# Kernel optimization log

Measured on AMD Instinct MI355X. Metric: run time of the kernel, lower is better.

## Reference

```python
import jax, jax.numpy as jnp
import numpy as np

B, H, C, N, K_TERMS = 256, 512, 64, 100, 8


def eval_cubic_spline(coeffs, tobs, t):
    # coeffs: [B, N-1, 4, C]; tobs: [N] sorted knots; t: scalar
    idx = jnp.clip(jnp.searchsorted(tobs, t, side='right') - 1, 0, tobs.shape[0] - 2)
    dt = t - tobs[idx]
    c = coeffs[:, idx]  # [B, 4, C]
    # Horner evaluation: c0 + c1*dt + c2*dt^2 + c3*dt^3
    return c[:, 0] + dt * (c[:, 1] + dt * (c[:, 2] + dt * c[:, 3]))


def setup_inputs() -> dict:
    key = jax.random.key(0)
    k_h, k_c, k_dc, k_wx, k_wh, k_wo = jax.random.split(key, 6)
    xav = lambda k, shape: jax.random.uniform(
        k, shape, minval=-1.0, maxval=1.0, dtype=jnp.float32
    ) * np.float32(np.sqrt(6.0 / (shape[0] + shape[1])))
    return {
        't': jnp.float32(0.5),
        'h': jax.random.normal(k_h, (B, H), dtype=jnp.float32),
        'coeffs': jax.random.normal(k_c, (B, N - 1, 4, C), dtype=jnp.float32),
        'dcoeffs': jax.random.normal(k_dc, (B, N - 1, 4, C), dtype=jnp.float32),
        'tobs': jnp.linspace(0.0, 1.0, N, dtype=jnp.float32),
        'wx': xav(k_wx, (H, C)),
        'wh': xav(k_wh, (H, H)),
        'wout': xav(k_wo, (H, H)),
        'b0': jnp.zeros((H,), dtype=jnp.float32),
        'b1': jnp.zeros((H,), dtype=jnp.float32),
    }


def reference(t, h, coeffs, dcoeffs, tobs, wx, wh, wout, b0, b1):
    x = eval_cubic_spline(coeffs, tobs, t)      # [B, C]
    xdot = eval_cubic_spline(dcoeffs, tobs, t)  # [B, C]
    l1 = x @ wx.T + h @ wh.T + b0               # [B, H]
    relu = jnp.maximum(l1, 0.0)
    th = jnp.tanh(relu @ wout.T + b1)           # [B, H]
    dtanh = 1.0 - th * th
    drelu = jax.nn.sigmoid(l1)                  # surrogate_relu branch
    # Jacobian assembly via broadcasted outer product: [B, H, H]
    d_outer = dtanh[:, :, None] * wout[None, :, :] * drelu[:, None, :]
    Jx = d_outer @ wx                           # [B, H, C]
    Jh = d_outer @ wh                           # [B, H, H]
    curr = jnp.einsum('bhc,bc->bh', Jx, xdot)   # jx matvec, [B, H]
    h_dot = curr
    for _ in range(K_TERMS):                    # Neumann-series recurrence
        curr = jnp.einsum('bij,bj->bi', Jh, curr)
        h_dot = h_dot + curr
    return h_dot
```

## Files before the change

### kernel.cpp

```cpp
#include <hip/hip_runtime.h>

#define BB 256
#define HH 512
#define CC 64
#define NN 100
#define KT 8

typedef short s16x8 __attribute__((ext_vector_type(8)));
typedef float f32x4 __attribute__((ext_vector_type(4)));

#define MFMA16(a, b, c) __builtin_amdgcn_mfma_f32_16x16x32_bf16((a), (b), (c), 0, 0, 0)

static __device__ __forceinline__ unsigned short f2bf(float f) {
    union { float f; unsigned int u; } v; v.f = f;
    unsigned int r = v.u + 0x7FFFu + ((v.u >> 16) & 1u);
    return (unsigned short)(r >> 16);
}


__global__ void k_pack(const float* __restrict__ wh, const float* __restrict__ wout,
                       const float* __restrict__ wx, const float* __restrict__ h,
                       const float* __restrict__ coeffs, const float* __restrict__ dcoeffs,
                       const float* __restrict__ tobs, const float* __restrict__ tg,
                       unsigned short* __restrict__ whp, unsigned short* __restrict__ wop,
                       unsigned short* __restrict__ wxp, unsigned short* __restrict__ hf,
                       unsigned short* __restrict__ xf, unsigned short* __restrict__ xdf) {
    int gid = blockIdx.x * 256 + threadIdx.x;
    if (gid < 524288) {
        const float* src = (gid < 262144) ? wh : wout;
        unsigned short* dst = (gid < 262144) ? whp : wop;
        int p = gid & 262143;
        int e = p & 7, lane = (p >> 3) & 63, g = (p >> 9) & 15, cg = (p >> 13) & 1, w = p >> 14;
        int row = w * 32 + cg * 16 + (lane & 15);
        int k = g * 32 + (lane >> 4) * 8 + e;
        dst[p] = f2bf(src[row * HH + k]);
    } else if (gid < 557056) {
        int p = gid - 524288;
        int e = p & 7, lane = (p >> 3) & 63, g = (p >> 9) & 1, cg = (p >> 10) & 1, w = p >> 11;
        int row = w * 32 + cg * 16 + (lane & 15);
        int k = g * 32 + (lane >> 4) * 8 + e;
        wxp[p] = f2bf(wx[row * CC + k]);
    } else if (gid < 688128) {
        int p = gid - 557056;
        int e = p & 7, lane = (p >> 3) & 63, g = (p >> 9) & 15, btp = p >> 13;
        int row = btp * 16 + (lane & 15);
        int k = g * 32 + (lane >> 4) * 8 + e;
        hf[p] = f2bf(h[row * HH + k]);
    } else if (gid < 704512) {
        int p = gid - 688128;
        int b = p >> 6, c = p & 63;
        float t = tg[0];
        int cntv = 0;
        for (int n = 0; n < NN; n++) cntv += (tobs[n] <= t) ? 1 : 0;
        int idx = cntv - 1;
        idx = idx < 0 ? 0 : (idx > NN - 2 ? NN - 2 : idx);
        float dt = t - tobs[idx];
        const float* cb = coeffs + ((size_t)(b * (NN - 1) + idx) * 4) * CC + c;
        float xv = cb[0] + dt * (cb[CC] + dt * (cb[2 * CC] + dt * cb[3 * CC]));
        const float* db = dcoeffs + ((size_t)(b * (NN - 1) + idx) * 4) * CC + c;
        float xd = db[0] + dt * (db[CC] + dt * (db[2 * CC] + dt * db[3 * CC]));
        int fi = (b >> 4) * 1024 + (c >> 5) * 512 + ((b & 15) + ((c >> 3) & 3) * 16) * 8 + (c & 7);
        xf[fi] = f2bf(xv);
        xdf[fi] = f2bf(xd);
    }
}

__global__ __launch_bounds__(512) void k_fused(
    const unsigned short* __restrict__ whp, const unsigned short* __restrict__ wop,
    const unsigned short* __restrict__ wxp, const unsigned short* __restrict__ hf,
    const unsigned short* __restrict__ xf, const unsigned short* __restrict__ xdf,
    const float* __restrict__ b0g, const float* __restrict__ b1g,
    float* __restrict__ outp) {
    __shared__ __align__(16) unsigned short sa[2][8192];
    const int tid = threadIdx.x;
    const int w = tid >> 6, lane = tid & 63;
    const int col2 = lane & 15, kq = lane >> 4;
    const int bt = blockIdx.x;

    float b0v[4], b1v[4];
    int fb[4];
#pragma unroll
    for (int t = 0; t < 4; t++) {
        const int c = (w * 4 + t) * 16 + col2;
        b0v[t] = b0g[c];
        b1v[t] = b1g[c];
        fb[t] = ((w * 4 + t) >> 1) * 512 + (col2 & 7) + (((t * 2 + (col2 >> 3)) & 3) << 7) + kq * 32;
    }

    const s16x8* wlh = (const s16x8*)whp + (size_t)w * 4096 + lane;
    const s16x8* wlo = (const s16x8*)wop + (size_t)w * 4096 + lane;

    float dr[4][4], dt[4][4], hd[4][4];

    {
        const s16x8* ha = (const s16x8*)(hf + (size_t)bt * 8192) + lane;
        f32x4 acc[4] = {{0.f, 0.f, 0.f, 0.f}, {0.f, 0.f, 0.f, 0.f},
                        {0.f, 0.f, 0.f, 0.f}, {0.f, 0.f, 0.f, 0.f}};
        f32x4 vac[4] = {{0.f, 0.f, 0.f, 0.f}, {0.f, 0.f, 0.f, 0.f},
                        {0.f, 0.f, 0.f, 0.f}, {0.f, 0.f, 0.f, 0.f}};
        s16x8 bfr[2][4], af[2];
        af[0] = ha[0];
#pragma unroll
        for (int t = 0; t < 4; t++) bfr[0][t] = wlh[t * 1024];
#pragma unroll
        for (int g = 0; g < 16; g++) {
            if (g < 15) {
                af[(g + 1) & 1] = ha[(g + 1) * 64];
#pragma unroll
                for (int t = 0; t < 4; t++) bfr[(g + 1) & 1][t] = wlh[t * 1024 + (g + 1) * 64];
            }
#pragma unroll
            for (int t = 0; t < 4; t++) acc[t] = MFMA16(af[g & 1], bfr[g & 1][t], acc[t]);
        }
#pragma unroll
        for (int g = 0; g < 2; g++) {
            const s16x8 xa = *((const s16x8*)(xf + (size_t)bt * 1024 + g * 512) + lane);
            const s16x8 xda = *((const s16x8*)(xdf + (size_t)bt * 1024 + g * 512) + lane);
#pragma unroll
            for (int t = 0; t < 4; t++) {
                const s16x8 bf = ((const s16x8*)wxp)[(size_t)((w * 4 + t) * 2 + g) * 64 + lane];
                acc[t] = MFMA16(xa, bf, acc[t]);
                vac[t] = MFMA16(xda, bf, vac[t]);
            }
        }
#pragma unroll
        for (int t = 0; t < 4; t++)
#pragma unroll
            for (int r = 0; r < 4; r++) {
                const float l1 = acc[t][r] + b0v[t];
                const float dra = 1.f / (1.f + expf(-l1));
                dr[t][r] = dra;
                sa[0][fb[t] + r * 8] = f2bf(fmaxf(l1, 0.f));
                sa[1][fb[t] + r * 8] = f2bf(dra * vac[t][r]);
            }
    }
    __syncthreads();

    {
        const unsigned short* A0 = &sa[0][lane * 8];
        const unsigned short* A1 = &sa[1][lane * 8];
        f32x4 acc[4] = {{0.f, 0.f, 0.f, 0.f}, {0.f, 0.f, 0.f, 0.f},
                        {0.f, 0.f, 0.f, 0.f}, {0.f, 0.f, 0.f, 0.f}};
        f32x4 cac[4] = {{0.f, 0.f, 0.f, 0.f}, {0.f, 0.f, 0.f, 0.f},
                        {0.f, 0.f, 0.f, 0.f}, {0.f, 0.f, 0.f, 0.f}};
        s16x8 bfr[2][4];
#pragma unroll
        for (int t = 0; t < 4; t++) bfr[0][t] = wlo[t * 1024];
#pragma unroll
        for (int g = 0; g < 16; g++) {
            if (g < 15) {
#pragma unroll
                for (int t = 0; t < 4; t++) bfr[(g + 1) & 1][t] = wlo[t * 1024 + (g + 1) * 64];
            }
            const s16x8 ar = *(const s16x8*)(A0 + (size_t)g * 512);
            const s16x8 as = *(const s16x8*)(A1 + (size_t)g * 512);
#pragma unroll
            for (int t = 0; t < 4; t++) {
                acc[t] = MFMA16(ar, bfr[g & 1][t], acc[t]);
                cac[t] = MFMA16(as, bfr[g & 1][t], cac[t]);
            }
        }
        __syncthreads();
#pragma unroll
        for (int t = 0; t < 4; t++)
#pragma unroll
            for (int r = 0; r < 4; r++) {
                const float th = tanhf(acc[t][r] + b1v[t]);
                const float dtv = 1.f - th * th;
                dt[t][r] = dtv;
                const float c0 = dtv * cac[t][r];
                hd[t][r] = c0;
                sa[0][fb[t] + r * 8] = f2bf(c0);
            }
    }
    __syncthreads();

    const unsigned short* A0 = &sa[0][lane * 8];
    const unsigned short* A1 = &sa[1][lane * 8];
    for (int p = 0; p < 16; p++) {
        const s16x8* wl = (p & 1) ? wlo : wlh;
        const unsigned short* Ar = (p & 1) ? A1 : A0;
        f32x4 acc[4] = {{0.f, 0.f, 0.f, 0.f}, {0.f, 0.f, 0.f, 0.f},
                        {0.f, 0.f, 0.f, 0.f}, {0.f, 0.f, 0.f, 0.f}};
        s16x8 bfr[2][4];
#pragma unroll
        for (int t = 0; t < 4; t++) bfr[0][t] = wl[t * 1024];
#pragma unroll
        for (int g = 0; g < 16; g++) {
            if (g < 15) {
#pragma unroll
                for (int t = 0; t < 4; t++) bfr[(g + 1) & 1][t] = wl[t * 1024 + (g + 1) * 64];
            }
            const s16x8 a = *(const s16x8*)(Ar + (size_t)g * 512);
#pragma unroll
            for (int t = 0; t < 4; t++) acc[t] = MFMA16(a, bfr[g & 1][t], acc[t]);
        }
        unsigned short* Aw = &sa[(p + 1) & 1][0];
        if (p & 1) {
            if (p < 15) {
#pragma unroll
                for (int t = 0; t < 4; t++)
#pragma unroll
                    for (int r = 0; r < 4; r++) {
                        float v = dt[t][r] * acc[t][r];
                        hd[t][r] += v;
                        Aw[fb[t] + r * 8] = f2bf(v);
                    }
            } else {
#pragma unroll
                for (int t = 0; t < 4; t++)
#pragma unroll
                    for (int r = 0; r < 4; r++) hd[t][r] += dt[t][r] * acc[t][r];
            }
        } else {
#pragma unroll
            for (int t = 0; t < 4; t++)
#pragma unroll
                for (int r = 0; r < 4; r++)
                    Aw[fb[t] + r * 8] = f2bf(dr[t][r] * acc[t][r]);
        }
        if (p < 15) __syncthreads();
    }

#pragma unroll
    for (int t = 0; t < 4; t++) {
        const int c = (w * 4 + t) * 16 + col2;
#pragma unroll
        for (int r = 0; r < 4; r++)
            outp[(size_t)(bt * 16 + kq * 4 + r) * HH + c] = hd[t][r];
    }
}

extern "C" void kernel_launch(void* const* d_in, const int* in_sizes, int n_in,
                              void* d_out, int out_size, void* d_ws, size_t ws_size,
                              hipStream_t stream) {
    const float* tg = (const float*)d_in[0];
    const float* h = (const float*)d_in[1];
    const float* coeffs = (const float*)d_in[2];
    const float* dcoeffs = (const float*)d_in[3];
    const float* tobs = (const float*)d_in[4];
    const float* wx = (const float*)d_in[5];
    const float* wh = (const float*)d_in[6];
    const float* wout = (const float*)d_in[7];
    const float* b0g = (const float*)d_in[8];
    const float* b1g = (const float*)d_in[9];
    float* outp = (float*)d_out;

    char* ws = (char*)d_ws;
    unsigned short* whp = (unsigned short*)(ws + 0);
    unsigned short* wop = (unsigned short*)(ws + 524288);
    unsigned short* wxp = (unsigned short*)(ws + 1048576);
    unsigned short* hf  = (unsigned short*)(ws + 1114112);
    unsigned short* xf  = (unsigned short*)(ws + 1376256);
    unsigned short* xdf = (unsigned short*)(ws + 1409024);

    k_pack<<<2752, 256, 0, stream>>>(wh, wout, wx, h, coeffs, dcoeffs, tobs, tg,
                                     whp, wop, wxp, hf, xf, xdf);
    k_fused<<<16, 512, 0, stream>>>(whp, wop, wxp, hf, xf, xdf, b0g, b1g, outp);
}
```

Baseline: 189.8 us.

## Pin last weight k-chunks in registers/LDS and prefetch next matmul's weights across stages

Result: slower. 337.8 us (+77.9%).

```diff
diff --git a/kernel.cpp b/kernel.cpp
--- a/kernel.cpp
+++ b/kernel.cpp
@@ -65,13 +65,114 @@
     }
 }
 
-__global__ __launch_bounds__(512) void k_fused(
+
+#define CORE1(WL, WLN, P13, P14, P15, WPI, AR) do {                              \
+    _Pragma("unroll")                                                            \
+    for (int t = 0; t < 4; t++) acc[t] = (f32x4){0.f, 0.f, 0.f, 0.f};            \
+    {                                                                            \
+        const s16x8 a12 = *(const s16x8*)((AR) + 12 * 512);                      \
+        const s16x8 a13 = *(const s16x8*)((AR) + 13 * 512);                      \
+        const s16x8 a14 = *(const s16x8*)((AR) + 14 * 512);                      \
+        const s16x8 a15 = *(const s16x8*)((AR) + 15 * 512);                      \
+        _Pragma("unroll")                                                        \
+        for (int t = 0; t < 4; t++) {                                            \
+            const s16x8 b12 = *(const s16x8*)&wpin[WPI][((w * 4 + t) * 64 + lane) * 8]; \
+            acc[t] = MFMA16(a12, b12, acc[t]);                                   \
+            acc[t] = MFMA16(a13, P13[t], acc[t]);                                \
+            acc[t] = MFMA16(a14, P14[t], acc[t]);                                \
+            acc[t] = MFMA16(a15, P15[t], acc[t]);                                \
+        }                                                                        \
+    }                                                                            \
+    _Pragma("unroll")                                                            \
+    for (int g = 0; g < 12; g += 2) {                                            \
+        {                                                                        \
+            const s16x8 a = *(const s16x8*)((AR) + g * 512);                     \
+            _Pragma("unroll")                                                    \
+            for (int t = 0; t < 4; t++) acc[t] = MFMA16(a, bfr0[t], acc[t]);     \
+            const s16x8* ws = (g < 10) ? (WL) : (WLN);                           \
+            const int gg = (g < 10) ? (g + 2) : (g - 10);                        \
+            _Pragma("unroll")                                                    \
+            for (int t = 0; t < 4; t++) bfr0[t] = ws[t * 1024 + gg * 64];        \
+        }                                                                        \
+        {                                                                        \
+            const s16x8 a = *(const s16x8*)((AR) + (g + 1) * 512);               \
+            _Pragma("unroll")                                                    \
+            for (int t = 0; t < 4; t++) acc[t] = MFMA16(a, bfr1[t], acc[t]);     \
+            const s16x8* ws = (g + 1 < 10) ? (WL) : (WLN);                       \
+            const int gg = (g + 1 < 10) ? (g + 3) : (g - 9);                     \
+            _Pragma("unroll")                                                    \
+            for (int t = 0; t < 4; t++) bfr1[t] = ws[t * 1024 + gg * 64];        \
+        }                                                                        \
+    }                                                                            \
+} while (0)
+
+#define CORE2(WL, WLN, P13, P14, P15, WPI, AR, AR2) do {                         \
+    _Pragma("unroll")                                                            \
+    for (int t = 0; t < 4; t++) {                                                \
+        acc[t] = (f32x4){0.f, 0.f, 0.f, 0.f};                                    \
+        cac[t] = (f32x4){0.f, 0.f, 0.f, 0.f};                                    \
+    }                                                                            \
+    {                                                                            \
+        const s16x8 a12 = *(const s16x8*)((AR) + 12 * 512);                      \
+        const s16x8 a13 = *(const s16x8*)((AR) + 13 * 512);                      \
+        const s16x8 a14 = *(const s16x8*)((AR) + 14 * 512);                      \
+        const s16x8 a15 = *(const s16x8*)((AR) + 15 * 512);                      \
+        const s16x8 c12 = *(const s16x8*)((AR2) + 12 * 512);                     \
+        const s16x8 c13 = *(const s16x8*)((AR2) + 13 * 512);                     \
+        const s16x8 c14 = *(const s16x8*)((AR2) + 14 * 512);                     \
+        const s16x8 c15 = *(const s16x8*)((AR2) + 15 * 512);                     \
+        _Pragma("unroll")                                                        \
+        for (int t = 0; t < 4; t++) {                                            \
+            const s16x8 b12 = *(const s16x8*)&wpin[WPI][((w * 4 + t) * 64 + lane) * 8]; \
+            acc[t] = MFMA16(a12, b12, acc[t]);                                   \
+            cac[t] = MFMA16(c12, b12, cac[t]);                                   \
+            acc[t] = MFMA16(a13, P13[t], acc[t]);                                \
+            cac[t] = MFMA16(c13, P13[t], cac[t]);                                \
+            acc[t] = MFMA16(a14, P14[t], acc[t]);                                \
+            cac[t] = MFMA16(c14, P14[t], cac[t]);                                \
+            acc[t] = MFMA16(a15, P15[t], acc[t]);                                \
+            cac[t] = MFMA16(c15, P15[t], cac[t]);                                \
+        }                                                                        \
+    }                                                                            \
+    _Pragma("unroll")                                                            \
+    for (int g = 0; g < 12; g += 2) {                                            \
+        {                                                                        \
+            const s16x8 a = *(const s16x8*)((AR) + g * 512);                     \
+            const s16x8 a2 = *(const s16x8*)((AR2) + g * 512);                   \
+            _Pragma("unroll")                                                    \
+            for (int t = 0; t < 4; t++) {                                        \
+                acc[t] = MFMA16(a, bfr0[t], acc[t]);                             \
+                cac[t] = MFMA16(a2, bfr0[t], cac[t]);                            \
+            }                                                                    \
+            const s16x8* ws = (g < 10) ? (WL) : (WLN);                           \
+            const int gg = (g < 10) ? (g + 2) : (g - 10);                        \
+            _Pragma("unroll")                                                    \
+            for (int t = 0; t < 4; t++) bfr0[t] = ws[t * 1024 + gg * 64];        \
+        }                                                                        \
+        {                                                                        \
+            const s16x8 a = *(const s16x8*)((AR) + (g + 1) * 512);               \
+            const s16x8 a2 = *(const s16x8*)((AR2) + (g + 1) * 512);             \
+            _Pragma("unroll")                                                    \
+            for (int t = 0; t < 4; t++) {                                        \
+                acc[t] = MFMA16(a, bfr1[t], acc[t]);                             \
+                cac[t] = MFMA16(a2, bfr1[t], cac[t]);                            \
+            }                                                                    \
+            const s16x8* ws = (g + 1 < 10) ? (WL) : (WLN);                       \
+            const int gg = (g + 1 < 10) ? (g + 3) : (g - 9);                     \
+            _Pragma("unroll")                                                    \
+            for (int t = 0; t < 4; t++) bfr1[t] = ws[t * 1024 + gg * 64];        \
+        }                                                                        \
+    }                                                                            \
+} while (0)
+
+__global__ __launch_bounds__(512, 2) void k_fused(
     const unsigned short* __restrict__ whp, const unsigned short* __restrict__ wop,
     const unsigned short* __restrict__ wxp, const unsigned short* __restrict__ hf,
     const unsigned short* __restrict__ xf, const unsigned short* __restrict__ xdf,
     const float* __restrict__ b0g, const float* __restrict__ b1g,
     float* __restrict__ outp) {
     __shared__ __align__(16) unsigned short sa[2][8192];
+    __shared__ __align__(16) unsigned short wpin[2][16384];
     const int tid = threadIdx.x;
     const int w = tid >> 6, lane = tid & 63;
     const int col2 = lane & 15, kq = lane >> 4;
@@ -90,39 +191,62 @@
     const s16x8* wlh = (const s16x8*)whp + (size_t)w * 4096 + lane;
     const s16x8* wlo = (const s16x8*)wop + (size_t)w * 4096 + lane;
 
+    {
+        const int4* src = (const int4*)(hf + (size_t)bt * 8192);
+        int4* dst = (int4*)&sa[0][0];
+        dst[tid] = src[tid];
+        dst[tid + 512] = src[tid + 512];
+    }
+#pragma unroll
+    for (int t = 0; t < 4; t++) {
+        *(s16x8*)&wpin[0][((w * 4 + t) * 64 + lane) * 8] = wlh[t * 1024 + 12 * 64];
+        *(s16x8*)&wpin[1][((w * 4 + t) * 64 + lane) * 8] = wlo[t * 1024 + 12 * 64];
+    }
+    s16x8 pnh13[4], pnh14[4], pnh15[4], pno13[4], pno14[4], pno15[4];
+#pragma unroll
+    for (int t = 0; t < 4; t++) {
+        pnh13[t] = wlh[t * 1024 + 13 * 64];
+        pnh14[t] = wlh[t * 1024 + 14 * 64];
+        pnh15[t] = wlh[t * 1024 + 15 * 64];
+        pno13[t] = wlo[t * 1024 + 13 * 64];
+        pno14[t] = wlo[t * 1024 + 14 * 64];
+        pno15[t] = wlo[t * 1024 + 15 * 64];
+    }
+    s16x8 xav[2], xdav[2], wxf[2][4];
+#pragma unroll
+    for (int g = 0; g < 2; g++) {
+        xav[g] = *((const s16x8*)(xf + (size_t)bt * 1024 + g * 512) + lane);
+        xdav[g] = *((const s16x8*)(xdf + (size_t)bt * 1024 + g * 512) + lane);
+#pragma unroll
+        for (int t = 0; t < 4; t++)
+            wxf[g][t] = ((const s16x8*)wxp)[(size_t)((w * 4 + t) * 2 + g) * 64 + lane];
+    }
+    s16x8 bfr0[4], bfr1[4];
+#pragma unroll
+    for (int t = 0; t < 4; t++) {
+        bfr0[t] = wlh[t * 1024];
+        bfr1[t] = wlh[t * 1024 + 64];
+    }
+
+    const unsigned short* A0 = &sa[0][lane * 8];
+    const unsigned short* A1 = &sa[1][lane * 8];
     float dr[4][4], dt[4][4], hd[4][4];
-
+    f32x4 acc[4], cac[4];
+
+    __syncthreads();
+
+    CORE1(wlh, wlo, pnh13, pnh14, pnh15, 0, A0);
     {
-        const s16x8* ha = (const s16x8*)(hf + (size_t)bt * 8192) + lane;
-        f32x4 acc[4] = {{0.f, 0.f, 0.f, 0.f}, {0.f, 0.f, 0.f, 0.f},
-                        {0.f, 0.f, 0.f, 0.f}, {0.f, 0.f, 0.f, 0.f}};
         f32x4 vac[4] = {{0.f, 0.f, 0.f, 0.f}, {0.f, 0.f, 0.f, 0.f},
                         {0.f, 0.f, 0.f, 0.f}, {0.f, 0.f, 0.f, 0.f}};
-        s16x8 bfr[2][4], af[2];
-        af[0] = ha[0];
-#pragma unroll
-        for (int t = 0; t < 4; t++) bfr[0][t] = wlh[t * 1024];
-#pragma unroll
-        for (int g = 0; g < 16; g++) {
-            if (g < 15) {
-                af[(g + 1) & 1] = ha[(g + 1) * 64];
-#pragma unroll
-                for (int t = 0; t < 4; t++) bfr[(g + 1) & 1][t] = wlh[t * 1024 + (g + 1) * 64];
+#pragma unroll
+        for (int g = 0; g < 2; g++)
+#pragma unroll
+            for (int t = 0; t < 4; t++) {
+                acc[t] = MFMA16(xav[g], wxf[g][t], acc[t]);
+                vac[t] = MFMA16(xdav[g], wxf[g][t], vac[t]);
             }
-#pragma unroll
-            for (int t = 0; t < 4; t++) acc[t] = MFMA16(af[g & 1], bfr[g & 1][t], acc[t]);
-        }
-#pragma unroll
-        for (int g = 0; g < 2; g++) {
-            const s16x8 xa = *((const s16x8*)(xf + (size_t)bt * 1024 + g * 512) + lane);
-            const s16x8 xda = *((const s16x8*)(xdf + (size_t)bt * 1024 + g * 512) + lane);
-#pragma unroll
-            for (int t = 0; t < 4; t++) {
-                const s16x8 bf = ((const s16x8*)wxp)[(size_t)((w * 4 + t) * 2 + g) * 64 + lane];
-                acc[t] = MFMA16(xa, bf, acc[t]);
-                vac[t] = MFMA16(xda, bf, vac[t]);
-            }
-        }
+        __syncthreads();
 #pragma unroll
         for (int t = 0; t < 4; t++)
 #pragma unroll
@@ -136,90 +260,47 @@
     }
     __syncthreads();
 
-    {
-        const unsigned short* A0 = &sa[0][lane * 8];
-        const unsigned short* A1 = &sa[1][lane * 8];
-        f32x4 acc[4] = {{0.f, 0.f, 0.f, 0.f}, {0.f, 0.f, 0.f, 0.f},
-                        {0.f, 0.f, 0.f, 0.f}, {0.f, 0.f, 0.f, 0.f}};
-        f32x4 cac[4] = {{0.f, 0.f, 0.f, 0.f}, {0.f, 0.f, 0.f, 0.f},
-                        {0.f, 0.f, 0.f, 0.f}, {0.f, 0.f, 0.f, 0.f}};
-        s16x8 bfr[2][4];
-#pragma unroll
-        for (int t = 0; t < 4; t++) bfr[0][t] = wlo[t * 1024];
-#pragma unroll
-        for (int g = 0; g < 16; g++) {
-            if (g < 15) {
-#pragma unroll
-                for (int t = 0; t < 4; t++) bfr[(g + 1) & 1][t] = wlo[t * 1024 + (g + 1) * 64];
-            }
-            const s16x8 ar = *(const s16x8*)(A0 + (size_t)g * 512);
-            const s16x8 as = *(const s16x8*)(A1 + (size_t)g * 512);
-#pragma unroll
-            for (int t = 0; t < 4; t++) {
-                acc[t] = MFMA16(ar, bfr[g & 1][t], acc[t]);
-                cac[t] = MFMA16(as, bfr[g & 1][t], cac[t]);
-            }
+    CORE2(wlo, wlh, pno13, pno14, pno15, 1, A0, A1);
+    __syncthreads();
+#pragma unroll
+    for (int t = 0; t < 4; t++)
+#pragma unroll
+        for (int r = 0; r < 4; r++) {
+            const float th = tanhf(acc[t][r] + b1v[t]);
+            const float dtv = 1.f - th * th;
+            dt[t][r] = dtv;
+            const float c0 = dtv * cac[t][r];
+            hd[t][r] = c0;
+            sa[0][fb[t] + r * 8] = f2bf(c0);
         }
+    __syncthreads();
+
+    for (int it = 0; it < 8; it++) {
+        CORE1(wlh, wlo, pnh13, pnh14, pnh15, 0, A0);
+#pragma unroll
+        for (int t = 0; t < 4; t++)
+#pragma unroll
+            for (int r = 0; r < 4; r++)
+                sa[1][fb[t] + r * 8] = f2bf(dr[t][r] * acc[t][r]);
         __syncthreads();
-#pragma unroll
-        for (int t = 0; t < 4; t++)
-#pragma unroll
-            for (int r = 0; r < 4; r++) {
-                const float th = tanhf(acc[t][r] + b1v[t]);
-                const float dtv = 1.f - th * th;
-                dt[t][r] = dtv;
-                const float c0 = dtv * cac[t][r];
-                hd[t][r] = c0;
-                sa[0][fb[t] + r * 8] = f2bf(c0);
-            }
-    }
-    __syncthreads();
-
-    const unsigned short* A0 = &sa[0][lane * 8];
-    const unsigned short* A1 = &sa[1][lane * 8];
-    for (int p = 0; p < 16; p++) {
-        const s16x8* wl = (p & 1) ? wlo : wlh;
-        const unsigned short* Ar = (p & 1) ? A1 : A0;
-        f32x4 acc[4] = {{0.f, 0.f, 0.f, 0.f}, {0.f, 0.f, 0.f, 0.f},
-                        {0.f, 0.f, 0.f, 0.f}, {0.f, 0.f, 0.f, 0.f}};
-        s16x8 bfr[2][4];
-#pragma unroll
-        for (int t = 0; t < 4; t++) bfr[0][t] = wl[t * 1024];
-#pragma unroll
-        for (int g = 0; g < 16; g++) {
-            if (g < 15) {
-#pragma unroll
-                for (int t = 0; t < 4; t++) bfr[(g + 1) & 1][t] = wl[t * 1024 + (g + 1) * 64];
-            }
-            const s16x8 a = *(const s16x8*)(Ar + (size_t)g * 512);
-#pragma unroll
-            for (int t = 0; t < 4; t++) acc[t] = MFMA16(a, bfr[g & 1][t], acc[t]);
+
+        CORE1(wlo, wlh, pno13, pno14, pno15, 1, A1);
+        if (it < 7) {
+#pragma unroll
+            for (int t = 0; t < 4; t++)
+#pragma unroll
+                for (int r = 0; r < 4; r++) {
+                    const float v = dt[t][r] * acc[t][r];
+                    hd[t][r] += v;
+                    sa[0][fb[t] + r * 8] = f2bf(v);
+                }
+            __syncthreads();
+        } else {
+#pragma unroll
+            for (int t = 0; t < 4; t++)
+#pragma unroll
+                for (int r = 0; r < 4; r++) hd[t][r] += dt[t][r] * acc[t][r];
         }
-        unsigned short* Aw = &sa[(p + 1) & 1][0];
-        if (p & 1) {
-            if (p < 15) {
-#pragma unroll
-                for (int t = 0; t < 4; t++)
-#pragma unroll
-                    for (int r = 0; r < 4; r++) {
-                        float v = dt[t][r] * acc[t][r];
-                        hd[t][r] += v;
-                        Aw[fb[t] + r * 8] = f2bf(v);
-                    }
-            } else {
-#pragma unroll
-                for (int t = 0; t < 4; t++)
-#pragma unroll
-                    for (int r = 0; r < 4; r++) hd[t][r] += dt[t][r] * acc[t][r];
-            }
-        } else {
-#pragma unroll
-            for (int t = 0; t < 4; t++)
-#pragma unroll
-                for (int r = 0; r < 4; r++)
-                    Aw[fb[t] + r * 8] = f2bf(dr[t][r] * acc[t][r]);
-        }
-        if (p < 15) __syncthreads();
     }
 
 #pragma unroll
```
